# Optimization experiments

Measured on AMD Instinct MI355X. Metric: run time of the kernel, lower is better.

## Reference

```python
import jax, jax.numpy as jnp
import numpy as np
import math

T = 0.28
EPS = 1e-06
D_MODEL = 1024
N_HEADS = 16
D_K = D_MODEL // N_HEADS


def compute_radius(t, epsilon):
    raw = math.sqrt(4.0 * t * math.log(1.0 / epsilon))
    return max(int(math.ceil(raw * 2.0)), 1)

RADIUS = compute_radius(T, EPS)  # = 8 for t=0.28, eps=1e-6
WIN = RADIUS + 1                 # causal band window: j in [i-RADIUS, i]


def setup_inputs() -> dict:
    key = jax.random.key(0)
    ks = jax.random.split(key, 5)
    B, S = 2, 4096
    x = jax.random.normal(ks[0], (B, S, D_MODEL), dtype=jnp.float32)
    scale = 1.0 / math.sqrt(D_MODEL)
    Wq = jax.random.normal(ks[1], (D_MODEL, D_MODEL), dtype=jnp.float32) * scale
    Wk = jax.random.normal(ks[2], (D_MODEL, D_MODEL), dtype=jnp.float32) * scale
    Wv = jax.random.normal(ks[3], (D_MODEL, D_MODEL), dtype=jnp.float32) * scale
    Wo = jax.random.normal(ks[4], (D_MODEL, D_MODEL), dtype=jnp.float32) * scale
    return {"x": x, "Wq": Wq, "Wk": Wk, "Wv": Wv, "Wo": Wo}


def reference(x, Wq, Wk, Wv, Wo):
    B, S, _ = x.shape

    def split_heads(h):  # (B,S,D) -> (B,H,S,dk)
        return h.reshape(B, S, N_HEADS, D_K).transpose(0, 2, 1, 3)

    q = split_heads(x @ Wq)
    k = split_heads(x @ Wk)
    v = split_heads(x @ Wv)

    # Banded causal attention: token i attends to j in [i-RADIUS, i].
    # This equals the full masked softmax in the torch reference because
    # all out-of-band / non-causal entries are -inf there.
    pos = jnp.arange(S)
    idx = pos[:, None] + jnp.arange(-RADIUS, 1)[None, :]
    valid = idx >= 0                                       # left boundary
    idx_c = jnp.clip(idx, 0, S - 1)

    k_win = k[:, :, idx_c, :]
    v_win = v[:, :, idx_c, :]

    scores = jnp.einsum('bhsd,bhswd->bhsw', q, k_win) / (2.0 * T)
    scores = jnp.where(valid[None, None, :, :], scores, -jnp.inf)
    wts = jax.nn.softmax(scores, axis=-1)
    wts = jnp.nan_to_num(wts, nan=0.0)  # diagonal always valid, but keep parity

    attn = jnp.einsum('bhsw,bhswd->bhsd', wts, v_win)      # (B,H,S,dk)
    attn = attn.transpose(0, 2, 1, 3).reshape(B, S, D_MODEL)
    return attn @ Wo
```

## Files before the change

kernel.cpp:

```cpp
#include <hip/hip_runtime.h>
#include <stdint.h>

constexpr int S_LEN = 4096;
constexpr int DM    = 1024;
constexpr int RAD   = 8;
constexpr float INV2T = 1.7857142857142858f;

constexpr int BM = 128, BN = 128, BK = 64;

typedef _Float16 h8v __attribute__((ext_vector_type(8)));
typedef float f32x4  __attribute__((ext_vector_type(4)));

static __device__ __forceinline__ void gl_lds16(const void* gp, void* lp) {
  auto g = (const __attribute__((address_space(1))) void*)(uintptr_t)gp;
  auto l = (__attribute__((address_space(3))) void*)(uint32_t)(uintptr_t)lp;
  __builtin_amdgcn_global_load_lds(g, l, 16, 0, 0);
}

__global__ __launch_bounds__(256) void sda_prep_kernel(
    const float* __restrict__ X, _Float16* __restrict__ XH,
    const float* __restrict__ W0, const float* __restrict__ W1,
    const float* __restrict__ W2, const float* __restrict__ W3,
    _Float16* __restrict__ T0, _Float16* __restrict__ T1,
    _Float16* __restrict__ T2, _Float16* __restrict__ T3) {
  __shared__ float t[32][33];
  int z = blockIdx.z;
  int tx = threadIdx.x, ty = threadIdx.y;
  if (z < 4) {
    const float* W = z == 0 ? W0 : (z == 1 ? W1 : (z == 2 ? W2 : W3));
    _Float16*    T = z == 0 ? T0 : (z == 1 ? T1 : (z == 2 ? T2 : T3));
    int n0 = blockIdx.x * 32, k0 = blockIdx.y * 32;
#pragma unroll
    for (int i = 0; i < 4; ++i)
      t[ty + 8 * i][tx] = W[(size_t)(k0 + ty + 8 * i) * DM + n0 + tx];
    __syncthreads();
#pragma unroll
    for (int i = 0; i < 4; ++i)
      T[(size_t)(n0 + ty + 8 * i) * DM + k0 + tx] = (_Float16)t[tx][ty + 8 * i];
  } else {
    int blk = (z - 4) * 1024 + blockIdx.y * 32 + blockIdx.x;
    int i = blk * 256 + ty * 32 + tx;
    const float4* x4 = (const float4*)X;
    float4 a = x4[2 * i], b = x4[2 * i + 1];
    float f[8] = {a.x, a.y, a.z, a.w, b.x, b.y, b.z, b.w};
    union { _Float16 h[8]; uint4 v; } o;
#pragma unroll
    for (int j = 0; j < 8; ++j) o.h[j] = (_Float16)f[j];
    ((uint4*)XH)[i] = o.v;
  }
}

__global__ __launch_bounds__(256) void sda_gemm_qkv_kernel(
    const _Float16* __restrict__ A, const _Float16* __restrict__ Bt,
    _Float16* __restrict__ C0, _Float16* __restrict__ C1,
    _Float16* __restrict__ C2) {
  constexpr int Kd = DM;
  __shared__ __align__(16) _Float16 As[BM * BK];
  __shared__ __align__(16) _Float16 Bs[BN * BK];

  int blk = blockIdx.x;
  int xcd = blk & 7, slot = blk >> 3;
  int xt = slot >> 3, ys = slot & 7;
  int yt = (xcd << 3) | ys;
  int m0 = yt * BM, n0 = xt * BN;

  int tid = threadIdx.x, wid = tid >> 6, lane = tid & 63;
  int srow = lane >> 3;
  int sgk = ((lane & 7) ^ (srow & 7)) * 8;
  int wm = (wid >> 1) * 64, wn = (wid & 1) * 64;
  int fm = lane & 15, fc = lane >> 4;

  f32x4 acc[4][4] = {};

  for (int kt = 0; kt < Kd / BK; ++kt) {
    if (kt) __syncthreads();
    int kk = kt * BK;
    int r0 = wid * 32;
#pragma unroll
    for (int i = 0; i < 4; ++i) {
      gl_lds16(A  + (size_t)(m0 + r0 + i * 8 + srow) * Kd + kk + sgk, &As[(r0 + i * 8) * BK]);
      gl_lds16(Bt + (size_t)(n0 + r0 + i * 8 + srow) * Kd + kk + sgk, &Bs[(r0 + i * 8) * BK]);
    }
    __syncthreads();

#pragma unroll
    for (int ks = 0; ks < 2; ++ks) {
      h8v af[4], bfr[4];
#pragma unroll
      for (int i = 0; i < 4; ++i) {
        int row = wm + i * 16 + fm;
        af[i] = *(const h8v*)&As[row * BK + (((ks * 4 + fc) ^ (row & 7)) * 8)];
      }
#pragma unroll
      for (int j = 0; j < 4; ++j) {
        int row = wn + j * 16 + fm;
        bfr[j] = *(const h8v*)&Bs[row * BK + (((ks * 4 + fc) ^ (row & 7)) * 8)];
      }
#pragma unroll
      for (int i = 0; i < 4; ++i)
#pragma unroll
        for (int j = 0; j < 4; ++j)
          acc[i][j] = __builtin_amdgcn_mfma_f32_16x16x32_f16(af[i], bfr[j], acc[i][j], 0, 0, 0);
    }
  }

  int which = n0 >> 10, nc = n0 & 1023;
  _Float16* Cv = which == 0 ? C0 : (which == 1 ? C1 : C2);

  int rr = (lane >> 4) * 4, cc = lane & 15;
#pragma unroll
  for (int i = 0; i < 4; ++i)
#pragma unroll
    for (int j = 0; j < 4; ++j) {
      size_t base = (size_t)(m0 + wm + i * 16 + rr) * DM + (nc + wn + j * 16 + cc);
#pragma unroll
      for (int r = 0; r < 4; ++r)
        Cv[base + (size_t)r * DM] = (_Float16)acc[i][j][r];
    }
}

__global__ __launch_bounds__(256) void sda_gemm_wo_kernel(
    const _Float16* __restrict__ A, const _Float16* __restrict__ Bt,
    float* __restrict__ C) {
  constexpr int Kd = DM;
  __shared__ __align__(16) _Float16 As[BM * BK];
  __shared__ __align__(16) _Float16 Bs[BN * BK];

  int blk = blockIdx.x;
  int xcd = blk & 7, slot = blk >> 3;
  int xt = slot >> 3, ys = slot & 7;
  int yt = (xcd << 3) | ys;
  int m0 = yt * BM, n0 = xt * BN;

  int tid = threadIdx.x, wid = tid >> 6, lane = tid & 63;
  int srow = lane >> 3;
  int sgk = ((lane & 7) ^ (srow & 7)) * 8;
  int wm = (wid >> 1) * 64, wn = (wid & 1) * 64;
  int fm = lane & 15, fc = lane >> 4;

  f32x4 acc[4][4] = {};

  for (int kt = 0; kt < Kd / BK; ++kt) {
    if (kt) __syncthreads();
    int kk = kt * BK;
    int r0 = wid * 32;
#pragma unroll
    for (int i = 0; i < 4; ++i) {
      gl_lds16(A  + (size_t)(m0 + r0 + i * 8 + srow) * Kd + kk + sgk, &As[(r0 + i * 8) * BK]);
      gl_lds16(Bt + (size_t)(n0 + r0 + i * 8 + srow) * Kd + kk + sgk, &Bs[(r0 + i * 8) * BK]);
    }
    __syncthreads();

#pragma unroll
    for (int ks = 0; ks < 2; ++ks) {
      h8v af[4], bfr[4];
#pragma unroll
      for (int i = 0; i < 4; ++i) {
        int row = wm + i * 16 + fm;
        af[i] = *(const h8v*)&As[row * BK + (((ks * 4 + fc) ^ (row & 7)) * 8)];
      }
#pragma unroll
      for (int j = 0; j < 4; ++j) {
        int row = wn + j * 16 + fm;
        bfr[j] = *(const h8v*)&Bs[row * BK + (((ks * 4 + fc) ^ (row & 7)) * 8)];
      }
#pragma unroll
      for (int i = 0; i < 4; ++i)
#pragma unroll
        for (int j = 0; j < 4; ++j)
          acc[i][j] = __builtin_amdgcn_mfma_f32_16x16x32_f16(af[i], bfr[j], acc[i][j], 0, 0, 0);
    }
  }

  int rr = (lane >> 4) * 4, cc = lane & 15;
#pragma unroll
  for (int i = 0; i < 4; ++i)
#pragma unroll
    for (int j = 0; j < 4; ++j) {
      size_t base = (size_t)(m0 + wm + i * 16 + rr) * DM + (n0 + wn + j * 16 + cc);
#pragma unroll
      for (int r = 0; r < 4; ++r)
        C[base + (size_t)r * DM] = acc[i][j][r];
    }
}

__global__ __launch_bounds__(256) void sda_attn_kernel(
    const _Float16* __restrict__ Q, const _Float16* __restrict__ K,
    const _Float16* __restrict__ V, _Float16* __restrict__ O) {
  constexpr int KS  = 72;
  constexpr int VTS = 40;
  constexpr int WS  = 40;
  __shared__ __align__(16) _Float16 kw[4][32 * KS];
  __shared__ __align__(16) _Float16 vt[4][64 * VTS];
  __shared__ __align__(16) float    sc[4][16 * 33];
  __shared__ __align__(16) _Float16 wt[4][16 * WS];

  int bh = blockIdx.y, b = bh >> 4, h = bh & 15;
  int s0 = blockIdx.x * 64;
  int tid = threadIdx.x, wid = tid >> 6, lane = tid & 63;
  size_t headoff = (size_t)b * S_LEN * DM + h * 64;

  _Float16* kwp = kw[wid];
  _Float16* vtp = vt[wid];
  float*    scp = sc[wid];
  _Float16* wtp = wt[wid];

  int p0 = s0 + wid * 16 - RAD;
  int fm = lane & 15, fkg = (lane >> 4) * 8;
  int rr = (lane >> 4) * 4, cc = lane & 15;

  {
    uint4 z = make_uint4(0, 0, 0, 0);
    ((uint4*)wtp)[lane] = z;
    if (lane < 16) ((uint4*)wtp)[64 + lane] = z;
    *(uint4*)&vtp[lane * VTS + 24] = z;
  }

#pragma unroll
  for (int i = 0; i < 3; ++i) {
    int item = i * 64 + lane;
    int row = item >> 3, ch = (item & 7) * 8;
    int pos = p0 + row;
    uint4 kv = make_uint4(0, 0, 0, 0);
    if (pos >= 0) kv = *(const uint4*)(K + headoff + (size_t)pos * DM + ch);
    *(uint4*)&kwp[row * KS + ch] = kv;
  }
#pragma unroll
  for (int i = 0; i < 3; ++i) {
    int item = i * 64 + lane;
    int row = item >> 3, chb = (item & 7) * 8;
    int pos = p0 + row;
    uint4 vv = make_uint4(0, 0, 0, 0);
    if (pos >= 0) vv = *(const uint4*)(V + headoff + (size_t)pos * DM + chb);
    union { uint4 v; _Float16 hh[8]; } u; u.v = vv;
#pragma unroll
    for (int d = 0; d < 8; ++d) vtp[(chb + d) * VTS + row] = u.hh[d];
  }

  const _Float16* qrow = Q + headoff + (size_t)(s0 + wid * 16 + fm) * DM;
  h8v aq0 = *(const h8v*)(qrow + fkg);
  h8v aq1 = *(const h8v*)(qrow + 32 + fkg);

  f32x4 accs[2] = {};
#pragma unroll
  for (int t = 0; t < 2; ++t) {
    h8v bk0 = *(const h8v*)&kwp[(t * 16 + fm) * KS + fkg];
    h8v bk1 = *(const h8v*)&kwp[(t * 16 + fm) * KS + 32 + fkg];
    accs[t] = __builtin_amdgcn_mfma_f32_16x16x32_f16(aq0, bk0, accs[t], 0, 0, 0);
    accs[t] = __builtin_amdgcn_mfma_f32_16x16x32_f16(aq1, bk1, accs[t], 0, 0, 0);
  }
#pragma unroll
  for (int t = 0; t < 2; ++t)
#pragma unroll
    for (int r = 0; r < 4; ++r)
      scp[(rr + r) * 33 + t * 16 + cc] = accs[t][r];

  if (lane < 16) {
    int r = lane, s = s0 + wid * 16 + r;
    const float* my = &scp[r * 33 + r];
    float e[9], mx = -1e30f;
#pragma unroll
    for (int j = 0; j < 9; ++j) {
      float p = my[j] * INV2T;
      e[j] = (s - RAD + j >= 0) ? p : -1e30f;
      mx = fmaxf(mx, e[j]);
    }
    float se = 0.f;
#pragma unroll
    for (int j = 0; j < 9; ++j) { e[j] = __expf(e[j] - mx); se += e[j]; }
    float inv = 1.f / se;
#pragma unroll
    for (int j = 0; j < 9; ++j)
      wtp[r * WS + r + j] = (_Float16)(e[j] * inv);
  }

  f32x4 acco[4] = {};
  h8v aw = *(const h8v*)&wtp[fm * WS + fkg];
#pragma unroll
  for (int t = 0; t < 4; ++t) {
    h8v bv = *(const h8v*)&vtp[(t * 16 + fm) * VTS + fkg];
    acco[t] = __builtin_amdgcn_mfma_f32_16x16x32_f16(aw, bv, acco[t], 0, 0, 0);
  }
#pragma unroll
  for (int t = 0; t < 4; ++t)
#pragma unroll
    for (int r = 0; r < 4; ++r)
      O[headoff + (size_t)(s0 + wid * 16 + rr + r) * DM + t * 16 + cc] =
          (_Float16)acco[t][r];
}

extern "C" void kernel_launch(void* const* d_in, const int* in_sizes, int n_in,
                              void* d_out, int out_size, void* d_ws, size_t ws_size,
                              hipStream_t stream) {
  (void)in_sizes; (void)n_in; (void)out_size; (void)ws_size;
  const float* x  = (const float*)d_in[0];
  const float* Wq = (const float*)d_in[1];
  const float* Wk = (const float*)d_in[2];
  const float* Wv = (const float*)d_in[3];
  const float* Wo = (const float*)d_in[4];

  char* ws = (char*)d_ws;
  const size_t MB = 1ull << 20;
  _Float16* xh    = (_Float16*)(ws + 0);
  _Float16* WqkvT = (_Float16*)(ws + 16 * MB);
  _Float16* WoT   = (_Float16*)(ws + 22 * MB);
  _Float16* Qh    = (_Float16*)(ws + 24 * MB);
  _Float16* Kh    = (_Float16*)(ws + 40 * MB);
  _Float16* Vh    = (_Float16*)(ws + 56 * MB);
  _Float16* Ah    = (_Float16*)(ws + 72 * MB);

  sda_prep_kernel<<<dim3(32, 32, 8), dim3(32, 8), 0, stream>>>(
      x, xh, Wq, Wk, Wv, Wo,
      WqkvT, WqkvT + (size_t)DM * DM, WqkvT + 2ull * DM * DM, WoT);

  sda_gemm_qkv_kernel<<<1536, 256, 0, stream>>>(xh, WqkvT, Qh, Kh, Vh);
  sda_attn_kernel<<<dim3(64, 32), 256, 0, stream>>>(Qh, Kh, Vh, Ah);
  sda_gemm_wo_kernel<<<512, 256, 0, stream>>>(Ah, WoT, (float*)d_out);
}
```

Before: 187.2 us.

## Replace GEMMs with triple-buffered 128x256 tile pipeline using 512 threads

Merges the QKV and output-projection GEMMs into one templated kernel. It uses 128x256 tiles with 8 waves and triple-buffered LDS, so global-to-LDS loads for step t+2 are issued while step t computes, with manual vmcnt waits and split barriers. It also raises MFMA priority with s_setprio. LDS use grows to about 144KB per block, which limits occupancy to one block per CU. The fewer, larger blocks change how the grid covers the CUs (768 and 256 blocks).

```diff
diff --git a/kernel.cpp b/kernel.cpp
--- a/kernel.cpp
+++ b/kernel.cpp
@@ -5,8 +5,6 @@
 constexpr int DM    = 1024;
 constexpr int RAD   = 8;
 constexpr float INV2T = 1.7857142857142858f;
-
-constexpr int BM = 128, BN = 128, BK = 64;
 
 typedef _Float16 h8v __attribute__((ext_vector_type(8)));
 typedef float f32x4  __attribute__((ext_vector_type(4)));
@@ -50,138 +48,117 @@
   }
 }
 
-__global__ __launch_bounds__(256) void sda_gemm_qkv_kernel(
+template <bool F32OUT>
+__global__ __launch_bounds__(512) void sda_gemm_pipe(
     const _Float16* __restrict__ A, const _Float16* __restrict__ Bt,
     _Float16* __restrict__ C0, _Float16* __restrict__ C1,
-    _Float16* __restrict__ C2) {
+    _Float16* __restrict__ C2, float* __restrict__ Cf) {
   constexpr int Kd = DM;
-  __shared__ __align__(16) _Float16 As[BM * BK];
-  __shared__ __align__(16) _Float16 Bs[BN * BK];
+  constexpr int NT = Kd / 64;
+  constexpr int ASZ = 128 * 64;
+  constexpr int BSZ = 256 * 64;
+  __shared__ __align__(16) _Float16 As[3][ASZ];
+  __shared__ __align__(16) _Float16 Bs[3][BSZ];
 
   int blk = blockIdx.x;
   int xcd = blk & 7, slot = blk >> 3;
   int xt = slot >> 3, ys = slot & 7;
   int yt = (xcd << 3) | ys;
-  int m0 = yt * BM, n0 = xt * BN;
+  int m0 = yt * 128, n0 = xt * 256;
 
   int tid = threadIdx.x, wid = tid >> 6, lane = tid & 63;
   int srow = lane >> 3;
-  int sgk = ((lane & 7) ^ (srow & 7)) * 8;
-  int wm = (wid >> 1) * 64, wn = (wid & 1) * 64;
+  int sgk = ((lane & 7) ^ srow) * 8;
+  int wm = (wid >> 2) * 64, wn = (wid & 3) * 64;
   int fm = lane & 15, fc = lane >> 4;
 
+  const _Float16* Ag = A  + (size_t)(m0 + 16 * wid + srow) * Kd + sgk;
+  const _Float16* Bg = Bt + (size_t)(n0 + 32 * wid + srow) * Kd + sgk;
+
   f32x4 acc[4][4] = {};
 
-  for (int kt = 0; kt < Kd / BK; ++kt) {
-    if (kt) __syncthreads();
-    int kk = kt * BK;
-    int r0 = wid * 32;
+  auto stage_g1 = [&](int buf, int kt) {
+    int kk = kt * 64;
+    gl_lds16(Ag + kk,           &As[buf][(16 * wid) * 64]);
+    gl_lds16(Ag + kk + 8 * Kd,  &As[buf][(16 * wid + 8) * 64]);
+    gl_lds16(Bg + kk,           &Bs[buf][(32 * wid) * 64]);
+  };
+  auto stage_g2 = [&](int buf, int kt) {
+    int kk = kt * 64;
+    gl_lds16(Bg + kk + 8 * Kd,  &Bs[buf][(32 * wid + 8) * 64]);
+    gl_lds16(Bg + kk + 16 * Kd, &Bs[buf][(32 * wid + 16) * 64]);
+    gl_lds16(Bg + kk + 24 * Kd, &Bs[buf][(32 * wid + 24) * 64]);
+  };
+
+  auto phase = [&](int buf, int kk) {
+    h8v a[4], b[4];
 #pragma unroll
     for (int i = 0; i < 4; ++i) {
-      gl_lds16(A  + (size_t)(m0 + r0 + i * 8 + srow) * Kd + kk + sgk, &As[(r0 + i * 8) * BK]);
-      gl_lds16(Bt + (size_t)(n0 + r0 + i * 8 + srow) * Kd + kk + sgk, &Bs[(r0 + i * 8) * BK]);
-    }
-    __syncthreads();
-
-#pragma unroll
-    for (int ks = 0; ks < 2; ++ks) {
-      h8v af[4], bfr[4];
-#pragma unroll
-      for (int i = 0; i < 4; ++i) {
-        int row = wm + i * 16 + fm;
-        af[i] = *(const h8v*)&As[row * BK + (((ks * 4 + fc) ^ (row & 7)) * 8)];
+      int row = wm + i * 16 + fm;
+      a[i] = *(const h8v*)&As[buf][row * 64 + (((kk * 4 + fc) ^ (row & 7)) * 8)];
+    }
+#pragma unroll
+    for (int j = 0; j < 4; ++j) {
+      int row = wn + j * 16 + fm;
+      b[j] = *(const h8v*)&Bs[buf][row * 64 + (((kk * 4 + fc) ^ (row & 7)) * 8)];
+    }
+    __builtin_amdgcn_s_setprio(1);
+#pragma unroll
+    for (int i = 0; i < 4; ++i)
+#pragma unroll
+      for (int j = 0; j < 4; ++j)
+        acc[i][j] = __builtin_amdgcn_mfma_f32_16x16x32_f16(a[i], b[j], acc[i][j], 0, 0, 0);
+    __builtin_amdgcn_s_setprio(0);
+  };
+
+  stage_g1(0, 0); stage_g2(0, 0);
+  stage_g1(1, 1); stage_g2(1, 1);
+
+  int cur = 0;
+#pragma unroll 1
+  for (int t = 0; t < NT; ++t) {
+    int nb = cur + 2; if (nb >= 3) nb -= 3;
+    if (t + 2 < NT) {
+      stage_g1(nb, t + 2);
+      asm volatile("s_waitcnt vmcnt(9)" ::: "memory");
+    } else if (t + 1 < NT) {
+      asm volatile("s_waitcnt vmcnt(6)" ::: "memory");
+    } else {
+      asm volatile("s_waitcnt vmcnt(0)" ::: "memory");
+    }
+    asm volatile("s_barrier" ::: "memory");
+    phase(cur, 0);
+    if (t + 2 < NT) stage_g2(nb, t + 2);
+    asm volatile("s_barrier" ::: "memory");
+    phase(cur, 1);
+    asm volatile("s_barrier" ::: "memory");
+    cur = cur == 2 ? 0 : cur + 1;
+  }
+
+  int rr = (lane >> 4) * 4, cc = lane & 15;
+  if constexpr (F32OUT) {
+#pragma unroll
+    for (int i = 0; i < 4; ++i)
+#pragma unroll
+      for (int j = 0; j < 4; ++j) {
+        size_t base = (size_t)(m0 + wm + i * 16 + rr) * DM + (n0 + wn + j * 16 + cc);
+#pragma unroll
+        for (int r = 0; r < 4; ++r)
+          Cf[base + (size_t)r * DM] = acc[i][j][r];
       }
+  } else {
+    int which = n0 >> 10, nc = n0 & 1023;
+    _Float16* Cv = which == 0 ? C0 : (which == 1 ? C1 : C2);
+#pragma unroll
+    for (int i = 0; i < 4; ++i)
 #pragma unroll
       for (int j = 0; j < 4; ++j) {
-        int row = wn + j * 16 + fm;
-        bfr[j] = *(const h8v*)&Bs[row * BK + (((ks * 4 + fc) ^ (row & 7)) * 8)];
+        size_t base = (size_t)(m0 + wm + i * 16 + rr) * DM + (nc + wn + j * 16 + cc);
+#pragma unroll
+        for (int r = 0; r < 4; ++r)
+          Cv[base + (size_t)r * DM] = (_Float16)acc[i][j][r];
       }
-#pragma unroll
-      for (int i = 0; i < 4; ++i)
-#pragma unroll
-        for (int j = 0; j < 4; ++j)
-          acc[i][j] = __builtin_amdgcn_mfma_f32_16x16x32_f16(af[i], bfr[j], acc[i][j], 0, 0, 0);
-    }
-  }
-
-  int which = n0 >> 10, nc = n0 & 1023;
-  _Float16* Cv = which == 0 ? C0 : (which == 1 ? C1 : C2);
-
-  int rr = (lane >> 4) * 4, cc = lane & 15;
-#pragma unroll
-  for (int i = 0; i < 4; ++i)
-#pragma unroll
-    for (int j = 0; j < 4; ++j) {
-      size_t base = (size_t)(m0 + wm + i * 16 + rr) * DM + (nc + wn + j * 16 + cc);
-#pragma unroll
-      for (int r = 0; r < 4; ++r)
-        Cv[base + (size_t)r * DM] = (_Float16)acc[i][j][r];
-    }
-}
-
-__global__ __launch_bounds__(256) void sda_gemm_wo_kernel(
-    const _Float16* __restrict__ A, const _Float16* __restrict__ Bt,
-    float* __restrict__ C) {
-  constexpr int Kd = DM;
-  __shared__ __align__(16) _Float16 As[BM * BK];
-  __shared__ __align__(16) _Float16 Bs[BN * BK];
-
-  int blk = blockIdx.x;
-  int xcd = blk & 7, slot = blk >> 3;
-  int xt = slot >> 3, ys = slot & 7;
-  int yt = (xcd << 3) | ys;
-  int m0 = yt * BM, n0 = xt * BN;
-
-  int tid = threadIdx.x, wid = tid >> 6, lane = tid & 63;
-  int srow = lane >> 3;
-  int sgk = ((lane & 7) ^ (srow & 7)) * 8;
-  int wm = (wid >> 1) * 64, wn = (wid & 1) * 64;
-  int fm = lane & 15, fc = lane >> 4;
-
-  f32x4 acc[4][4] = {};
-
-  for (int kt = 0; kt < Kd / BK; ++kt) {
-    if (kt) __syncthreads();
-    int kk = kt * BK;
-    int r0 = wid * 32;
-#pragma unroll
-    for (int i = 0; i < 4; ++i) {
-      gl_lds16(A  + (size_t)(m0 + r0 + i * 8 + srow) * Kd + kk + sgk, &As[(r0 + i * 8) * BK]);
-      gl_lds16(Bt + (size_t)(n0 + r0 + i * 8 + srow) * Kd + kk + sgk, &Bs[(r0 + i * 8) * BK]);
-    }
-    __syncthreads();
-
-#pragma unroll
-    for (int ks = 0; ks < 2; ++ks) {
-      h8v af[4], bfr[4];
-#pragma unroll
-      for (int i = 0; i < 4; ++i) {
-        int row = wm + i * 16 + fm;
-        af[i] = *(const h8v*)&As[row * BK + (((ks * 4 + fc) ^ (row & 7)) * 8)];
-      }
-#pragma unroll
-      for (int j = 0; j < 4; ++j) {
-        int row = wn + j * 16 + fm;
-        bfr[j] = *(const h8v*)&Bs[row * BK + (((ks * 4 + fc) ^ (row & 7)) * 8)];
-      }
-#pragma unroll
-      for (int i = 0; i < 4; ++i)
-#pragma unroll
-        for (int j = 0; j < 4; ++j)
-          acc[i][j] = __builtin_amdgcn_mfma_f32_16x16x32_f16(af[i], bfr[j], acc[i][j], 0, 0, 0);
-    }
-  }
-
-  int rr = (lane >> 4) * 4, cc = lane & 15;
-#pragma unroll
-  for (int i = 0; i < 4; ++i)
-#pragma unroll
-    for (int j = 0; j < 4; ++j) {
-      size_t base = (size_t)(m0 + wm + i * 16 + rr) * DM + (n0 + wn + j * 16 + cc);
-#pragma unroll
-      for (int r = 0; r < 4; ++r)
-        C[base + (size_t)r * DM] = acc[i][j][r];
-    }
+  }
 }
 
 __global__ __launch_bounds__(256) void sda_attn_kernel(
@@ -313,7 +290,7 @@
       x, xh, Wq, Wk, Wv, Wo,
       WqkvT, WqkvT + (size_t)DM * DM, WqkvT + 2ull * DM * DM, WoT);
 
-  sda_gemm_qkv_kernel<<<1536, 256, 0, stream>>>(xh, WqkvT, Qh, Kh, Vh);
+  sda_gemm_pipe<false><<<768, 512, 0, stream>>>(xh, WqkvT, Qh, Kh, Vh, nullptr);
   sda_attn_kernel<<<dim3(64, 32), 256, 0, stream>>>(Qh, Kh, Vh, Ah);
-  sda_gemm_wo_kernel<<<512, 256, 0, stream>>>(Ah, WoT, (float*)d_out);
-}
+  sda_gemm_pipe<true><<<256, 512, 0, stream>>>(Ah, WoT, nullptr, nullptr, nullptr, (float*)d_out);
+}
```

Result: slower. 199.8 us (+6.7%).

## Rewrite QKV GEMM with 256x192 tiles and double-buffered LDS pipeline

Applied to the files above, without the earlier changes.

The QKV projection GEMM now uses 512-thread blocks with 256x192 tiles, double-buffered LDS, and async global-to-LDS prefetch of the next K-tile. This prefetch is interleaved with four MFMA phases per iteration using explicit waitcnt, barriers and setprio. Output is written to one fused QKV buffer with row stride 3072, and the attention kernel reads Q/K/V through offsets into that buffer. The aim is to hide load latency and raise MFMA utilisation. The cost is much higher register and LDS pressure (about 112KB LDS per block) and fewer blocks (512).

```diff
diff --git a/kernel.cpp b/kernel.cpp
--- a/kernel.cpp
+++ b/kernel.cpp
@@ -4,9 +4,8 @@
 constexpr int S_LEN = 4096;
 constexpr int DM    = 1024;
 constexpr int RAD   = 8;
+constexpr int NQKV  = 3072;
 constexpr float INV2T = 1.7857142857142858f;
-
-constexpr int BM = 128, BN = 128, BK = 64;
 
 typedef _Float16 h8v __attribute__((ext_vector_type(8)));
 typedef float f32x4  __attribute__((ext_vector_type(4)));
@@ -50,79 +49,126 @@
   }
 }
 
-__global__ __launch_bounds__(256) void sda_gemm_qkv_kernel(
+__global__ __launch_bounds__(512, 2) void sda_gemm_qkv_pipe(
     const _Float16* __restrict__ A, const _Float16* __restrict__ Bt,
-    _Float16* __restrict__ C0, _Float16* __restrict__ C1,
-    _Float16* __restrict__ C2) {
+    _Float16* __restrict__ C) {
   constexpr int Kd = DM;
-  __shared__ __align__(16) _Float16 As[BM * BK];
-  __shared__ __align__(16) _Float16 Bs[BN * BK];
+  constexpr int NT = Kd / 64;
+  __shared__ __align__(16) _Float16 As[2][256 * 64];
+  __shared__ __align__(16) _Float16 Bs[2][192 * 64];
 
   int blk = blockIdx.x;
   int xcd = blk & 7, slot = blk >> 3;
-  int xt = slot >> 3, ys = slot & 7;
-  int yt = (xcd << 3) | ys;
-  int m0 = yt * BM, n0 = xt * BN;
+  int xt = slot & 15, yq = slot >> 4;
+  int yt = (xcd << 2) | yq;
+  int m0 = yt * 256, n0 = xt * 192;
 
   int tid = threadIdx.x, wid = tid >> 6, lane = tid & 63;
   int srow = lane >> 3;
-  int sgk = ((lane & 7) ^ (srow & 7)) * 8;
-  int wm = (wid >> 1) * 64, wn = (wid & 1) * 64;
+  int sgk = ((lane & 7) ^ srow) * 8;
+  int wm = (wid >> 2) * 128, wn = (wid & 3) * 48;
   int fm = lane & 15, fc = lane >> 4;
 
-  f32x4 acc[4][4] = {};
-
-  for (int kt = 0; kt < Kd / BK; ++kt) {
-    if (kt) __syncthreads();
-    int kk = kt * BK;
-    int r0 = wid * 32;
-#pragma unroll
-    for (int i = 0; i < 4; ++i) {
-      gl_lds16(A  + (size_t)(m0 + r0 + i * 8 + srow) * Kd + kk + sgk, &As[(r0 + i * 8) * BK]);
-      gl_lds16(Bt + (size_t)(n0 + r0 + i * 8 + srow) * Kd + kk + sgk, &Bs[(r0 + i * 8) * BK]);
-    }
-    __syncthreads();
-
-#pragma unroll
-    for (int ks = 0; ks < 2; ++ks) {
-      h8v af[4], bfr[4];
-#pragma unroll
-      for (int i = 0; i < 4; ++i) {
-        int row = wm + i * 16 + fm;
-        af[i] = *(const h8v*)&As[row * BK + (((ks * 4 + fc) ^ (row & 7)) * 8)];
+  const _Float16* Ar = A  + (size_t)(m0 + 8 * wid + srow) * Kd + sgk;
+  const _Float16* Br = Bt + (size_t)(n0 + 8 * wid + srow) * Kd + sgk;
+
+  f32x4 acc[8][3] = {};
+
+#define STA(buf, kt, s) \
+  gl_lds16(Ar + (size_t)(64 * (s)) * Kd + (kt) * 64, &As[buf][(64 * (s) + 8 * wid) * 64])
+#define STB(buf, kt, s) \
+  gl_lds16(Br + (size_t)(64 * (s)) * Kd + (kt) * 64, &Bs[buf][(64 * (s) + 8 * wid) * 64])
+
+#define LDA4(af, cbuf, mh, ks)                                              \
+  _Pragma("unroll") for (int i = 0; i < 4; ++i) {                           \
+    int row = wm + (mh) * 64 + i * 16 + fm;                                 \
+    af[i] = *(const h8v*)&As[cbuf][row * 64 + ((((ks) * 4 + fc) ^ (row & 7)) * 8)]; \
+  }
+#define LDB3(bf, cbuf, ks)                                                  \
+  _Pragma("unroll") for (int j = 0; j < 3; ++j) {                           \
+    int row = wn + j * 16 + fm;                                             \
+    bf[j] = *(const h8v*)&Bs[cbuf][row * 64 + ((((ks) * 4 + fc) ^ (row & 7)) * 8)]; \
+  }
+#define MFMA12(af, bf, mh)                                                  \
+  __builtin_amdgcn_s_setprio(1);                                            \
+  _Pragma("unroll") for (int i = 0; i < 4; ++i)                             \
+  _Pragma("unroll") for (int j = 0; j < 3; ++j)                             \
+    acc[(mh) * 4 + i][j] =                                                  \
+        __builtin_amdgcn_mfma_f32_16x16x32_f16(af[i], bf[j], acc[(mh) * 4 + i][j], 0, 0, 0); \
+  __builtin_amdgcn_s_setprio(0);
+#define BARRIER asm volatile("s_barrier" ::: "memory")
+
+  STA(0, 0, 0); STA(0, 0, 1); STB(0, 0, 0); STB(0, 0, 1); STB(0, 0, 2);
+  STA(0, 0, 2); STA(0, 0, 3);
+  asm volatile("s_waitcnt vmcnt(2)" ::: "memory");
+  BARRIER;
+
+#pragma unroll 1
+  for (int t = 0; t < NT; ++t) {
+    int c = t & 1, nb = c ^ 1;
+    bool pre = (t + 1 < NT);
+    {
+      h8v af[4], bf[3];
+      LDA4(af, c, 0, 0); LDB3(bf, c, 0);
+      if (pre) {
+        STA(nb, t + 1, 0); STA(nb, t + 1, 1);
+        STB(nb, t + 1, 0); STB(nb, t + 1, 1); STB(nb, t + 1, 2);
+        asm volatile("s_waitcnt vmcnt(5)" ::: "memory");
+      } else {
+        asm volatile("s_waitcnt vmcnt(0)" ::: "memory");
       }
-#pragma unroll
-      for (int j = 0; j < 4; ++j) {
-        int row = wn + j * 16 + fm;
-        bfr[j] = *(const h8v*)&Bs[row * BK + (((ks * 4 + fc) ^ (row & 7)) * 8)];
-      }
-#pragma unroll
-      for (int i = 0; i < 4; ++i)
-#pragma unroll
-        for (int j = 0; j < 4; ++j)
-          acc[i][j] = __builtin_amdgcn_mfma_f32_16x16x32_f16(af[i], bfr[j], acc[i][j], 0, 0, 0);
-    }
-  }
-
-  int which = n0 >> 10, nc = n0 & 1023;
-  _Float16* Cv = which == 0 ? C0 : (which == 1 ? C1 : C2);
+      BARRIER;
+      MFMA12(af, bf, 0);
+      BARRIER;
+    }
+    {
+      h8v af[4], bf[3];
+      LDA4(af, c, 1, 0); LDB3(bf, c, 0);
+      if (pre) { STA(nb, t + 1, 2); STA(nb, t + 1, 3); }
+      BARRIER;
+      MFMA12(af, bf, 1);
+      BARRIER;
+    }
+    {
+      h8v af[4], bf[3];
+      LDA4(af, c, 0, 1); LDB3(bf, c, 1);
+      BARRIER;
+      MFMA12(af, bf, 0);
+      BARRIER;
+    }
+    {
+      h8v af[4], bf[3];
+      LDA4(af, c, 1, 1); LDB3(bf, c, 1);
+      if (pre) asm volatile("s_waitcnt vmcnt(2)" ::: "memory");
+      BARRIER;
+      MFMA12(af, bf, 1);
+      BARRIER;
+    }
+  }
 
   int rr = (lane >> 4) * 4, cc = lane & 15;
 #pragma unroll
-  for (int i = 0; i < 4; ++i)
-#pragma unroll
-    for (int j = 0; j < 4; ++j) {
-      size_t base = (size_t)(m0 + wm + i * 16 + rr) * DM + (nc + wn + j * 16 + cc);
+  for (int i = 0; i < 8; ++i)
+#pragma unroll
+    for (int j = 0; j < 3; ++j) {
+      size_t base = (size_t)(m0 + wm + i * 16 + rr) * NQKV + (n0 + wn + j * 16 + cc);
 #pragma unroll
       for (int r = 0; r < 4; ++r)
-        Cv[base + (size_t)r * DM] = (_Float16)acc[i][j][r];
-    }
+        C[base + (size_t)r * NQKV] = (_Float16)acc[i][j][r];
+    }
+#undef STA
+#undef STB
+#undef LDA4
+#undef LDB3
+#undef MFMA12
+#undef BARRIER
 }
 
 __global__ __launch_bounds__(256) void sda_gemm_wo_kernel(
     const _Float16* __restrict__ A, const _Float16* __restrict__ Bt,
     float* __restrict__ C) {
   constexpr int Kd = DM;
+  constexpr int BM = 128, BN = 128, BK = 64;
   __shared__ __align__(16) _Float16 As[BM * BK];
   __shared__ __align__(16) _Float16 Bs[BN * BK];
 
@@ -198,7 +244,8 @@
   int bh = blockIdx.y, b = bh >> 4, h = bh & 15;
   int s0 = blockIdx.x * 64;
   int tid = threadIdx.x, wid = tid >> 6, lane = tid & 63;
-  size_t headoff = (size_t)b * S_LEN * DM + h * 64;
+  size_t qkvoff = (size_t)b * S_LEN * NQKV + h * 64;
+  size_t ooff   = (size_t)b * S_LEN * DM   + h * 64;
 
   _Float16* kwp = kw[wid];
   _Float16* vtp = vt[wid];
@@ -222,7 +269,7 @@
     int row = item >> 3, ch = (item & 7) * 8;
     int pos = p0 + row;
     uint4 kv = make_uint4(0, 0, 0, 0);
-    if (pos >= 0) kv = *(const uint4*)(K + headoff + (size_t)pos * DM + ch);
+    if (pos >= 0) kv = *(const uint4*)(K + qkvoff + (size_t)pos * NQKV + ch);
     *(uint4*)&kwp[row * KS + ch] = kv;
   }
 #pragma unroll
@@ -231,13 +278,13 @@
     int row = item >> 3, chb = (item & 7) * 8;
     int pos = p0 + row;
     uint4 vv = make_uint4(0, 0, 0, 0);
-    if (pos >= 0) vv = *(const uint4*)(V + headoff + (size_t)pos * DM + chb);
+    if (pos >= 0) vv = *(const uint4*)(V + qkvoff + (size_t)pos * NQKV + chb);
     union { uint4 v; _Float16 hh[8]; } u; u.v = vv;
 #pragma unroll
     for (int d = 0; d < 8; ++d) vtp[(chb + d) * VTS + row] = u.hh[d];
   }
 
-  const _Float16* qrow = Q + headoff + (size_t)(s0 + wid * 16 + fm) * DM;
+  const _Float16* qrow = Q + qkvoff + (size_t)(s0 + wid * 16 + fm) * NQKV;
   h8v aq0 = *(const h8v*)(qrow + fkg);
   h8v aq1 = *(const h8v*)(qrow + 32 + fkg);
 
@@ -285,7 +332,7 @@
   for (int t = 0; t < 4; ++t)
 #pragma unroll
     for (int r = 0; r < 4; ++r)
-      O[headoff + (size_t)(s0 + wid * 16 + rr + r) * DM + t * 16 + cc] =
+      O[ooff + (size_t)(s0 + wid * 16 + rr + r) * DM + t * 16 + cc] =
           (_Float16)acco[t][r];
 }
 
@@ -304,16 +351,15 @@
   _Float16* xh    = (_Float16*)(ws + 0);
   _Float16* WqkvT = (_Float16*)(ws + 16 * MB);
   _Float16* WoT   = (_Float16*)(ws + 22 * MB);
-  _Float16* Qh    = (_Float16*)(ws + 24 * MB);
-  _Float16* Kh    = (_Float16*)(ws + 40 * MB);
-  _Float16* Vh    = (_Float16*)(ws + 56 * MB);
+  _Float16* QKVh  = (_Float16*)(ws + 24 * MB);
   _Float16* Ah    = (_Float16*)(ws + 72 * MB);
 
   sda_prep_kernel<<<dim3(32, 32, 8), dim3(32, 8), 0, stream>>>(
       x, xh, Wq, Wk, Wv, Wo,
       WqkvT, WqkvT + (size_t)DM * DM, WqkvT + 2ull * DM * DM, WoT);
 
-  sda_gemm_qkv_kernel<<<1536, 256, 0, stream>>>(xh, WqkvT, Qh, Kh, Vh);
-  sda_attn_kernel<<<dim3(64, 32), 256, 0, stream>>>(Qh, Kh, Vh, Ah);
+  sda_gemm_qkv_pipe<<<512, 512, 0, stream>>>(xh, WqkvT, QKVh);
+  sda_attn_kernel<<<dim3(64, 32), 256, 0, stream>>>(
+      QKVh, QKVh + 1024, QKVh + 2048, Ah);
   sda_gemm_wo_kernel<<<512, 256, 0, stream>>>(Ah, WoT, (float*)d_out);
 }
```

New measurement: 192.3 us. +2.7%, slower.
